# Kernel tuning notes

Measured on AMD Instinct MI355X. Metric: run time of the kernel, lower is better.

## Reference

```python
import jax, jax.numpy as jnp
import numpy as np

N_NODES = 50000
N_EDGES = 800000
IN_F = 128
H_F = 128
OUT_F = 128
N_GRAPHS = 128


def setup_inputs() -> dict:
    key = jax.random.key(0)
    ks = jax.random.split(key, 7)
    x = jax.random.normal(ks[0], (N_NODES, IN_F), dtype=jnp.float32)
    edge_index = jax.random.randint(ks[1], (2, N_EDGES), 0, N_NODES, dtype=jnp.int32)
    batch = jnp.sort(jax.random.randint(ks[2], (N_NODES,), 0, N_GRAPHS, dtype=jnp.int32))
    s1 = 1.0 / np.sqrt(IN_F)
    s2 = 1.0 / np.sqrt(H_F)
    W1 = jax.random.uniform(ks[3], (IN_F, H_F), jnp.float32, -s1, s1)
    b1 = jnp.zeros((H_F,), jnp.float32)
    W2 = jax.random.uniform(ks[4], (H_F, OUT_F), jnp.float32, -s2, s2)
    b2 = jnp.zeros((OUT_F,), jnp.float32)
    return {"x": x, "edge_index": edge_index, "batch": batch,
            "W1": W1, "b1": b1, "W2": W2, "b2": b2}


def _gcn_conv(x, W, b, src, dst, n_nodes):
    # PyG GCNConv: out = D^{-1/2} (A + I) D^{-1/2} (x W) + b
    h = x @ W  # [N, out]
    # degree including self-loop
    deg = jax.ops.segment_sum(jnp.ones_like(dst, dtype=h.dtype), dst,
                              num_segments=n_nodes) + 1.0
    dinv = jax.lax.rsqrt(deg)  # [N]
    norm = dinv[src] * dinv[dst]  # [E]
    agg = jax.ops.segment_sum(h[src] * norm[:, None], dst, num_segments=n_nodes)
    # self-loop term has norm dinv[i]^2
    return agg + (dinv * dinv)[:, None] * h + b


def reference(x, edge_index, batch, W1, b1, W2, b2):
    src, dst = edge_index[0], edge_index[1]
    h = jax.nn.relu(_gcn_conv(x, W1, b1, src, dst, N_NODES))
    h = _gcn_conv(h, W2, b2, src, dst, N_NODES)
    # global_add_pool over graphs
    return jax.ops.segment_sum(h, batch, num_segments=N_GRAPHS)
```

## Files before the change

### kernel.cpp

```cpp
#include <hip/hip_runtime.h>
#include <hip/hip_bf16.h>


typedef _Float16 f16x8 __attribute__((ext_vector_type(8)));
typedef float f32x4 __attribute__((ext_vector_type(4)));

#define BCHUNK 4096

static __device__ __forceinline__ float f16lo(unsigned int u) {
    union { unsigned short s; _Float16 h; } c; c.s = (unsigned short)(u & 0xffff);
    return (float)c.h;
}
static __device__ __forceinline__ float f16hi(unsigned int u) {
    union { unsigned short s; _Float16 h; } c; c.s = (unsigned short)(u >> 16);
    return (float)c.h;
}
static __device__ __forceinline__ unsigned int pack2f16(float x, float y) {
    union { unsigned short s; _Float16 h; } a, b;
    a.h = (_Float16)x; b.h = (_Float16)y;
    return (unsigned int)a.s | ((unsigned int)b.s << 16);
}


__global__ __launch_bounds__(256) void bin_hist(const int* __restrict__ ei,
                                                int* __restrict__ counts,
                                                int E, int NB, int NBLK) {
    __shared__ int hist[256];
    int t = threadIdx.x, blk = blockIdx.x;
    for (int b = t; b < NB; b += 256) hist[b] = 0;
    __syncthreads();
    int base = blk * BCHUNK;
    int end = min(E, base + BCHUNK);
    for (int e = base + t; e < end; e += 256)
        atomicAdd(&hist[ei[E + e] >> 8], 1);
    __syncthreads();
    for (int b = t; b < NB; b += 256) counts[b * NBLK + blk] = hist[b];
}

__global__ __launch_bounds__(256) void bin_scatter(const int* __restrict__ ei,
                                                   const int* __restrict__ counts,
                                                   unsigned int* __restrict__ bedges,
                                                   int E, int NB, int NBLK) {
    __shared__ int lcur[256];
    int t = threadIdx.x, blk = blockIdx.x;
    for (int b = t; b < NB; b += 256) lcur[b] = counts[b * NBLK + blk];
    __syncthreads();
    int base = blk * BCHUNK;
    int end = min(E, base + BCHUNK);
    for (int e = base + t; e < end; e += 256) {
        int s = ei[e];
        int d = ei[E + e];
        int pos = atomicAdd(&lcur[d >> 8], 1);
        bedges[pos] = (unsigned int)s | ((unsigned int)(d & 255) << 16);
    }
}

__global__ __launch_bounds__(256) void deg_buckets(const unsigned int* __restrict__ bedges,
                                                   const int* __restrict__ counts,
                                                   int* __restrict__ cnt,
                                                   int E, int N, int NB, int NBLK) {
    __shared__ int lcnt[256];
    int b = blockIdx.x, t = threadIdx.x;
    lcnt[t] = 0;
    __syncthreads();
    int bstart = counts[b * NBLK];
    int bend = (b + 1 < NB) ? counts[(b + 1) * NBLK] : E;
    for (int i = bstart + t; i < bend; i += 256)
        atomicAdd(&lcnt[bedges[i] >> 16], 1);
    __syncthreads();
    int node = (b << 8) + t;
    if (node < N) cnt[node] = lcnt[t];
}

__global__ __launch_bounds__(256) void fill_buckets(const unsigned int* __restrict__ bedges,
                                                    const int* __restrict__ counts,
                                                    const int* __restrict__ row_start,
                                                    int* __restrict__ srcs,
                                                    int E, int N, int NB, int NBLK) {
    __shared__ int lcur[256];
    int b = blockIdx.x, t = threadIdx.x;
    int node = (b << 8) + t;
    lcur[t] = (node < N) ? row_start[node] : 0;
    __syncthreads();
    int bstart = counts[b * NBLK];
    int bend = (b + 1 < NB) ? counts[(b + 1) * NBLK] : E;
    for (int i = bstart + t; i < bend; i += 256) {
        unsigned int p = bedges[i];
        int pos = atomicAdd(&lcur[p >> 16], 1);
        srcs[pos] = (int)(p & 0xffffu);
    }
}


__global__ void block_sums(const int* __restrict__ data, int* __restrict__ bsum, int n) {
    __shared__ int s[256];
    int base = blockIdx.x * 1024;
    int t = threadIdx.x;
    int v = 0;
#pragma unroll
    for (int i = 0; i < 4; i++) {
        int idx = base + t * 4 + i;
        if (idx < n) v += data[idx];
    }
    s[t] = v;
    __syncthreads();
    for (int off = 128; off > 0; off >>= 1) {
        if (t < off) s[t] += s[t + off];
        __syncthreads();
    }
    if (t == 0) bsum[blockIdx.x] = s[0];
}

__global__ void scan_bsum(int* __restrict__ bsum, int nb) {
    int lane = threadIdx.x & 63;
    int v = (lane < nb) ? bsum[lane] : 0;
    int incl = v;
#pragma unroll
    for (int off = 1; off < 64; off *= 2) {
        int u = __shfl_up(incl, off);
        if (lane >= off) incl += u;
    }
    if (lane < nb) bsum[lane] = incl - v;
}

__global__ void scan_apply(int* __restrict__ data, const int* __restrict__ bsum, int n) {
    __shared__ int s[256];
    int base = blockIdx.x * 1024;
    int t = threadIdx.x;
    int loc[4];
    int v = 0;
#pragma unroll
    for (int i = 0; i < 4; i++) {
        int idx = base + t * 4 + i;
        loc[i] = (idx < n) ? data[idx] : 0;
        v += loc[i];
    }
    s[t] = v;
    __syncthreads();
    for (int off = 1; off < 256; off *= 2) {
        int u = (t >= off) ? s[t - off] : 0;
        __syncthreads();
        s[t] += u;
        __syncthreads();
    }
    int excl = s[t] - v + bsum[blockIdx.x];
#pragma unroll
    for (int i = 0; i < 4; i++) {
        int idx = base + t * 4 + i;
        if (idx < n) { data[idx] = excl; excl += loc[i]; }
    }
}

__global__ void scan_nodes(const int* __restrict__ cnt, const int* __restrict__ bsum,
                           int* __restrict__ row_start, float* __restrict__ dinv, int n) {
    __shared__ int s[256];
    int base = blockIdx.x * 1024;
    int t = threadIdx.x;
    int loc[4];
    int v = 0;
#pragma unroll
    for (int i = 0; i < 4; i++) {
        int idx = base + t * 4 + i;
        loc[i] = (idx < n) ? cnt[idx] : 0;
        v += loc[i];
    }
    s[t] = v;
    __syncthreads();
    for (int off = 1; off < 256; off *= 2) {
        int u = (t >= off) ? s[t - off] : 0;
        __syncthreads();
        s[t] += u;
        __syncthreads();
    }
    int excl = s[t] - v + bsum[blockIdx.x];
#pragma unroll
    for (int i = 0; i < 4; i++) {
        int idx = base + t * 4 + i;
        if (idx < n) {
            row_start[idx] = excl;
            dinv[idx] = rsqrtf((float)loc[i] + 1.0f);
            excl += loc[i];
        }
    }
}

__global__ void wprep(const float* __restrict__ W, _Float16* __restrict__ wfrag) {
    int idx = blockIdx.x * 256 + threadIdx.x;
    if (idx >= 2048) return;
    int lane = idx & 63;
    int kc = (idx >> 6) & 3;
    int nb = idx >> 8;
    int col = nb * 16 + (lane & 15);
    int krow = kc * 32 + (lane >> 4) * 8;
#pragma unroll
    for (int j = 0; j < 8; j++)
        wfrag[idx * 8 + j] = (_Float16)W[(krow + j) * 128 + col];
}

template <bool A_IS_F32>
__global__ __launch_bounds__(256) void gemm_mfma(const void* __restrict__ Av,
                                                 const _Float16* __restrict__ wfrag,
                                                 _Float16* __restrict__ C, int M) {
    __shared__ _Float16 As[128 * 136];
    int t = threadIdx.x;
    int row0 = blockIdx.x * 128;

    if (A_IS_F32) {
        const float4* A4 = (const float4*)Av;
#pragma unroll
        for (int it = 0; it < 16; it++) {
            int v = it * 256 + t;
            int row = v >> 5;
            int seg = v & 31;
            float4 val = make_float4(0.f, 0.f, 0.f, 0.f);
            if (row0 + row < M) val = A4[(size_t)(row0 + row) * 32 + seg];
            _Float16* p = &As[row * 136 + seg * 4];
            p[0] = (_Float16)val.x; p[1] = (_Float16)val.y;
            p[2] = (_Float16)val.z; p[3] = (_Float16)val.w;
        }
    } else {
        const uint4* A4 = (const uint4*)Av;
#pragma unroll
        for (int it = 0; it < 8; it++) {
            int v = it * 256 + t;
            int row = v >> 4;
            int seg = v & 15;
            uint4 val = make_uint4(0, 0, 0, 0);
            if (row0 + row < M) val = A4[(size_t)(row0 + row) * 16 + seg];
            *((uint4*)&As[row * 136 + seg * 8]) = val;
        }
    }
    __syncthreads();

    int wv = t >> 6;
    int lane = t & 63;
    int lrow = lane & 15;
    int lq = lane >> 4;

    f32x4 acc[2][8];
#pragma unroll
    for (int i = 0; i < 2; i++)
#pragma unroll
        for (int j = 0; j < 8; j++) acc[i][j] = (f32x4){0.f, 0.f, 0.f, 0.f};

#pragma unroll
    for (int kc = 0; kc < 4; kc++) {
        int k0 = kc * 32;
        f16x8 a0 = *((const f16x8*)&As[(wv * 32 + lrow) * 136 + k0 + lq * 8]);
        f16x8 a1 = *((const f16x8*)&As[(wv * 32 + 16 + lrow) * 136 + k0 + lq * 8]);
#pragma unroll
        for (int nb = 0; nb < 8; nb++) {
            f16x8 b = ((const f16x8*)wfrag)[(nb * 4 + kc) * 64 + lane];
            acc[0][nb] = __builtin_amdgcn_mfma_f32_16x16x32_f16(a0, b, acc[0][nb], 0, 0, 0);
            acc[1][nb] = __builtin_amdgcn_mfma_f32_16x16x32_f16(a1, b, acc[1][nb], 0, 0, 0);
        }
    }

#pragma unroll
    for (int ti = 0; ti < 2; ti++) {
#pragma unroll
        for (int r = 0; r < 4; r++) {
            int row = row0 + wv * 32 + ti * 16 + lq * 4 + r;
            if (row < M) {
#pragma unroll
                for (int nb = 0; nb < 8; nb++)
                    C[(size_t)row * 128 + nb * 16 + lrow] = (_Float16)acc[ti][nb][r];
            }
        }
    }
}

template <bool RELU>
__global__ __launch_bounds__(256) void agg(const _Float16* __restrict__ hb,
                                           const int* __restrict__ srcs,
                                           const int* __restrict__ row_start,
                                           const int* __restrict__ cnt,
                                           const float* __restrict__ dinv,
                                           const float* __restrict__ bias,
                                           _Float16* __restrict__ ob, int n) {
    int node = blockIdx.x * 4 + (threadIdx.x >> 6);
    if (node >= n) return;
    int lane = threadIdx.x & 63;
    int s0 = row_start[node];
    int c = cnt[node];
    float dn = dinv[node];
    const unsigned int* h2 = (const unsigned int*)hb;
    float ax = 0.f, ay = 0.f, bx = 0.f, by = 0.f;
    int e = 0;
    for (; e + 8 <= c; e += 8) {
        int s0i = srcs[s0 + e + 0];
        int s1i = srcs[s0 + e + 1];
        int s2i = srcs[s0 + e + 2];
        int s3i = srcs[s0 + e + 3];
        int s4i = srcs[s0 + e + 4];
        int s5i = srcs[s0 + e + 5];
        int s6i = srcs[s0 + e + 6];
        int s7i = srcs[s0 + e + 7];
        float d0 = dinv[s0i], d1 = dinv[s1i], d2 = dinv[s2i], d3 = dinv[s3i];
        float d4 = dinv[s4i], d5 = dinv[s5i], d6 = dinv[s6i], d7 = dinv[s7i];
        unsigned int v0 = h2[(size_t)s0i * 64 + lane];
        unsigned int v1 = h2[(size_t)s1i * 64 + lane];
        unsigned int v2 = h2[(size_t)s2i * 64 + lane];
        unsigned int v3 = h2[(size_t)s3i * 64 + lane];
        unsigned int v4 = h2[(size_t)s4i * 64 + lane];
        unsigned int v5 = h2[(size_t)s5i * 64 + lane];
        unsigned int v6 = h2[(size_t)s6i * 64 + lane];
        unsigned int v7 = h2[(size_t)s7i * 64 + lane];
        float w0 = d0 * dn, w1 = d1 * dn, w2 = d2 * dn, w3 = d3 * dn;
        float w4 = d4 * dn, w5 = d5 * dn, w6 = d6 * dn, w7 = d7 * dn;
        ax = fmaf(w0, f16lo(v0), ax); ay = fmaf(w0, f16hi(v0), ay);
        bx = fmaf(w1, f16lo(v1), bx); by = fmaf(w1, f16hi(v1), by);
        ax = fmaf(w2, f16lo(v2), ax); ay = fmaf(w2, f16hi(v2), ay);
        bx = fmaf(w3, f16lo(v3), bx); by = fmaf(w3, f16hi(v3), by);
        ax = fmaf(w4, f16lo(v4), ax); ay = fmaf(w4, f16hi(v4), ay);
        bx = fmaf(w5, f16lo(v5), bx); by = fmaf(w5, f16hi(v5), by);
        ax = fmaf(w6, f16lo(v6), ax); ay = fmaf(w6, f16hi(v6), ay);
        bx = fmaf(w7, f16lo(v7), bx); by = fmaf(w7, f16hi(v7), by);
    }
    for (; e + 4 <= c; e += 4) {
        int s0i = srcs[s0 + e + 0];
        int s1i = srcs[s0 + e + 1];
        int s2i = srcs[s0 + e + 2];
        int s3i = srcs[s0 + e + 3];
        float d0 = dinv[s0i], d1 = dinv[s1i], d2 = dinv[s2i], d3 = dinv[s3i];
        unsigned int v0 = h2[(size_t)s0i * 64 + lane];
        unsigned int v1 = h2[(size_t)s1i * 64 + lane];
        unsigned int v2 = h2[(size_t)s2i * 64 + lane];
        unsigned int v3 = h2[(size_t)s3i * 64 + lane];
        float w0 = d0 * dn, w1 = d1 * dn, w2 = d2 * dn, w3 = d3 * dn;
        ax = fmaf(w0, f16lo(v0), ax); ay = fmaf(w0, f16hi(v0), ay);
        bx = fmaf(w1, f16lo(v1), bx); by = fmaf(w1, f16hi(v1), by);
        ax = fmaf(w2, f16lo(v2), ax); ay = fmaf(w2, f16hi(v2), ay);
        bx = fmaf(w3, f16lo(v3), bx); by = fmaf(w3, f16hi(v3), by);
    }
    for (; e < c; e++) {
        int si = srcs[s0 + e];
        float w = dinv[si] * dn;
        unsigned int v = h2[(size_t)si * 64 + lane];
        ax = fmaf(w, f16lo(v), ax); ay = fmaf(w, f16hi(v), ay);
    }
    ax += bx; ay += by;
    float sw = dn * dn;
    unsigned int hs = h2[(size_t)node * 64 + lane];
    float2 bv = ((const float2*)bias)[lane];
    float ox = ax + sw * f16lo(hs) + bv.x;
    float oy = ay + sw * f16hi(hs) + bv.y;
    if (RELU) { ox = fmaxf(ox, 0.f); oy = fmaxf(oy, 0.f); }
    ((unsigned int*)ob)[(size_t)node * 64 + lane] = pack2f16(ox, oy);
}

#define POOL_CHUNK 128
__global__ __launch_bounds__(256) void pool2h(const _Float16* __restrict__ feat,
                                              const int* __restrict__ batch,
                                              float* __restrict__ out, int n) {
    int wave = threadIdx.x >> 6;
    int lane = threadIdx.x & 63;
    int base = blockIdx.x * POOL_CHUNK;
    int end = base + POOL_CHUNK;
    if (end > n) end = n;
    const unsigned int* f2 = (const unsigned int*)feat;
    float accx = 0.f, accy = 0.f;
    int cur_g = -1;
    for (int i = base + wave; i < end; i += 4) {
        int g = batch[i];
        if (g != cur_g) {
            if (cur_g >= 0) {
                atomicAdd(&out[cur_g * 128 + lane * 2 + 0], accx);
                atomicAdd(&out[cur_g * 128 + lane * 2 + 1], accy);
            }
            cur_g = g;
            accx = 0.f; accy = 0.f;
        }
        unsigned int v = f2[(size_t)i * 64 + lane];
        accx += f16lo(v);
        accy += f16hi(v);
    }
    if (cur_g >= 0) {
        atomicAdd(&out[cur_g * 128 + lane * 2 + 0], accx);
        atomicAdd(&out[cur_g * 128 + lane * 2 + 1], accy);
    }
}

extern "C" void kernel_launch(void* const* d_in, const int* in_sizes, int n_in,
                              void* d_out, int out_size, void* d_ws, size_t ws_size,
                              hipStream_t stream) {
    const float* x  = (const float*)d_in[0];
    const int*   ei = (const int*)d_in[1];
    const int*   batch = (const int*)d_in[2];
    const float* W1 = (const float*)d_in[3];
    const float* b1 = (const float*)d_in[4];
    const float* W2 = (const float*)d_in[5];
    const float* b2 = (const float*)d_in[6];
    float* out = (float*)d_out;

    const int N = in_sizes[2];
    const int E = in_sizes[1] / 2;

    const int NB = (N + 255) >> 8;
    const int NBLK = (E + BCHUNK - 1) / BCHUNK;
    const int ncounts = NB * NBLK;

    _Float16* hb = (_Float16*)d_ws;
    _Float16* ob = hb + (size_t)N * 128;
    int* cnt  = (int*)(ob + (size_t)N * 128);
    int* row_start = cnt + N;
    float* dinv    = (float*)(row_start + N);
    int* srcs      = (int*)(dinv + N);
    unsigned int* bedges = (unsigned int*)(srcs + E);
    int* counts    = (int*)(bedges + E);
    _Float16* wfrag1 = (_Float16*)(counts + ncounts);
    _Float16* wfrag2 = wfrag1 + 128 * 128;
    int* bsum      = (int*)(wfrag2 + 128 * 128);

    const int nbc = (ncounts + 1023) / 1024;
    const int nbn = (N + 1023) / 1024;

    hipMemsetAsync(out, 0, (size_t)out_size * sizeof(float), stream);
    wprep<<<8, 256, 0, stream>>>(W1, wfrag1);
    wprep<<<8, 256, 0, stream>>>(W2, wfrag2);

    bin_hist<<<NBLK, 256, 0, stream>>>(ei, counts, E, NB, NBLK);
    block_sums<<<nbc, 256, 0, stream>>>(counts, bsum, ncounts);
    scan_bsum<<<1, 64, 0, stream>>>(bsum, nbc);
    scan_apply<<<nbc, 256, 0, stream>>>(counts, bsum, ncounts);
    bin_scatter<<<NBLK, 256, 0, stream>>>(ei, counts, bedges, E, NB, NBLK);
    deg_buckets<<<NB, 256, 0, stream>>>(bedges, counts, cnt, E, N, NB, NBLK);
    block_sums<<<nbn, 256, 0, stream>>>(cnt, bsum, N);
    scan_bsum<<<1, 64, 0, stream>>>(bsum, nbn);
    scan_nodes<<<nbn, 256, 0, stream>>>(cnt, bsum, row_start, dinv, N);
    fill_buckets<<<NB, 256, 0, stream>>>(bedges, counts, row_start, srcs, E, N, NB, NBLK);

    const int gemm_grid = (N + 127) / 128;

    gemm_mfma<true><<<gemm_grid, 256, 0, stream>>>(x, wfrag1, hb, N);
    agg<true><<<(N + 3) / 4, 256, 0, stream>>>(hb, srcs, row_start, cnt, dinv, b1, ob, N);
    gemm_mfma<false><<<gemm_grid, 256, 0, stream>>>(ob, wfrag2, hb, N);
    agg<false><<<(N + 3) / 4, 256, 0, stream>>>(hb, srcs, row_start, cnt, dinv, b2, ob, N);
    pool2h<<<(N + POOL_CHUNK - 1) / POOL_CHUNK, 256, 0, stream>>>(ob, batch, out, N);
}
```

Measured before the change: 241.2 us.

## Reorder second GCN layer: aggregate and pool before applying W2

Exploits linearity of the second layer. It aggregates the layer-1 output over neighbours, pools per graph into a small 128x128 buffer, and only then multiplies by W2 and adds bias scaled by node count per graph. This removes the full N x 128 x 128 second GEMM and the separate pool pass, fusing aggregation with pooling. Pooling now uses block-level shared-memory reduction plus atomics. Accumulation happens in fp32 before the weight multiply, which slightly changes rounding order.

```diff
diff --git a/kernel.cpp b/kernel.cpp
--- a/kernel.cpp
+++ b/kernel.cpp
@@ -197,38 +197,24 @@
         wfrag[idx * 8 + j] = (_Float16)W[(krow + j) * 128 + col];
 }
 
-template <bool A_IS_F32>
-__global__ __launch_bounds__(256) void gemm_mfma(const void* __restrict__ Av,
-                                                 const _Float16* __restrict__ wfrag,
-                                                 _Float16* __restrict__ C, int M) {
+__global__ __launch_bounds__(256) void gemm_mfma_f32in(const float* __restrict__ A,
+                                                       const _Float16* __restrict__ wfrag,
+                                                       _Float16* __restrict__ C, int M) {
     __shared__ _Float16 As[128 * 136];
     int t = threadIdx.x;
     int row0 = blockIdx.x * 128;
 
-    if (A_IS_F32) {
-        const float4* A4 = (const float4*)Av;
-#pragma unroll
-        for (int it = 0; it < 16; it++) {
-            int v = it * 256 + t;
-            int row = v >> 5;
-            int seg = v & 31;
-            float4 val = make_float4(0.f, 0.f, 0.f, 0.f);
-            if (row0 + row < M) val = A4[(size_t)(row0 + row) * 32 + seg];
-            _Float16* p = &As[row * 136 + seg * 4];
-            p[0] = (_Float16)val.x; p[1] = (_Float16)val.y;
-            p[2] = (_Float16)val.z; p[3] = (_Float16)val.w;
-        }
-    } else {
-        const uint4* A4 = (const uint4*)Av;
-#pragma unroll
-        for (int it = 0; it < 8; it++) {
-            int v = it * 256 + t;
-            int row = v >> 4;
-            int seg = v & 15;
-            uint4 val = make_uint4(0, 0, 0, 0);
-            if (row0 + row < M) val = A4[(size_t)(row0 + row) * 16 + seg];
-            *((uint4*)&As[row * 136 + seg * 8]) = val;
-        }
+    const float4* A4 = (const float4*)A;
+#pragma unroll
+    for (int it = 0; it < 16; it++) {
+        int v = it * 256 + t;
+        int row = v >> 5;
+        int seg = v & 31;
+        float4 val = make_float4(0.f, 0.f, 0.f, 0.f);
+        if (row0 + row < M) val = A4[(size_t)(row0 + row) * 32 + seg];
+        _Float16* p = &As[row * 136 + seg * 4];
+        p[0] = (_Float16)val.x; p[1] = (_Float16)val.y;
+        p[2] = (_Float16)val.z; p[3] = (_Float16)val.w;
     }
     __syncthreads();
 
@@ -270,14 +256,13 @@
     }
 }
 
-template <bool RELU>
-__global__ __launch_bounds__(256) void agg(const _Float16* __restrict__ hb,
-                                           const int* __restrict__ srcs,
-                                           const int* __restrict__ row_start,
-                                           const int* __restrict__ cnt,
-                                           const float* __restrict__ dinv,
-                                           const float* __restrict__ bias,
-                                           _Float16* __restrict__ ob, int n) {
+__global__ __launch_bounds__(256) void agg1(const _Float16* __restrict__ hb,
+                                            const int* __restrict__ srcs,
+                                            const int* __restrict__ row_start,
+                                            const int* __restrict__ cnt,
+                                            const float* __restrict__ dinv,
+                                            const float* __restrict__ bias,
+                                            _Float16* __restrict__ ob, int n) {
     int node = blockIdx.x * 4 + (threadIdx.x >> 6);
     if (node >= n) return;
     int lane = threadIdx.x & 63;
@@ -345,40 +330,127 @@
     float2 bv = ((const float2*)bias)[lane];
     float ox = ax + sw * f16lo(hs) + bv.x;
     float oy = ay + sw * f16hi(hs) + bv.y;
-    if (RELU) { ox = fmaxf(ox, 0.f); oy = fmaxf(oy, 0.f); }
+    ox = fmaxf(ox, 0.f); oy = fmaxf(oy, 0.f);
     ((unsigned int*)ob)[(size_t)node * 64 + lane] = pack2f16(ox, oy);
 }
 
-#define POOL_CHUNK 128
-__global__ __launch_bounds__(256) void pool2h(const _Float16* __restrict__ feat,
-                                              const int* __restrict__ batch,
-                                              float* __restrict__ out, int n) {
-    int wave = threadIdx.x >> 6;
+__global__ __launch_bounds__(256) void agg2_pool(const _Float16* __restrict__ ob,
+                                                 const int* __restrict__ srcs,
+                                                 const int* __restrict__ row_start,
+                                                 const int* __restrict__ cnt,
+                                                 const float* __restrict__ dinv,
+                                                 const int* __restrict__ batch,
+                                                 float* __restrict__ P, int n) {
+    __shared__ float red[4][128];
+    int wv = threadIdx.x >> 6;
     int lane = threadIdx.x & 63;
-    int base = blockIdx.x * POOL_CHUNK;
-    int end = base + POOL_CHUNK;
-    if (end > n) end = n;
-    const unsigned int* f2 = (const unsigned int*)feat;
-    float accx = 0.f, accy = 0.f;
-    int cur_g = -1;
-    for (int i = base + wave; i < end; i += 4) {
-        int g = batch[i];
-        if (g != cur_g) {
-            if (cur_g >= 0) {
-                atomicAdd(&out[cur_g * 128 + lane * 2 + 0], accx);
-                atomicAdd(&out[cur_g * 128 + lane * 2 + 1], accy);
-            }
-            cur_g = g;
-            accx = 0.f; accy = 0.f;
-        }
-        unsigned int v = f2[(size_t)i * 64 + lane];
-        accx += f16lo(v);
-        accy += f16hi(v);
-    }
-    if (cur_g >= 0) {
-        atomicAdd(&out[cur_g * 128 + lane * 2 + 0], accx);
-        atomicAdd(&out[cur_g * 128 + lane * 2 + 1], accy);
-    }
+    int base = blockIdx.x * 4;
+    int node = base + wv;
+    const unsigned int* h2 = (const unsigned int*)ob;
+    float ax = 0.f, ay = 0.f, bx = 0.f, by = 0.f;
+    int g = -1;
+    if (node < n) {
+        g = batch[node];
+        int s0 = row_start[node];
+        int c = cnt[node];
+        float dn = dinv[node];
+        int e = 0;
+        for (; e + 8 <= c; e += 8) {
+            int s0i = srcs[s0 + e + 0];
+            int s1i = srcs[s0 + e + 1];
+            int s2i = srcs[s0 + e + 2];
+            int s3i = srcs[s0 + e + 3];
+            int s4i = srcs[s0 + e + 4];
+            int s5i = srcs[s0 + e + 5];
+            int s6i = srcs[s0 + e + 6];
+            int s7i = srcs[s0 + e + 7];
+            float d0 = dinv[s0i], d1 = dinv[s1i], d2 = dinv[s2i], d3 = dinv[s3i];
+            float d4 = dinv[s4i], d5 = dinv[s5i], d6 = dinv[s6i], d7 = dinv[s7i];
+            unsigned int v0 = h2[(size_t)s0i * 64 + lane];
+            unsigned int v1 = h2[(size_t)s1i * 64 + lane];
+            unsigned int v2 = h2[(size_t)s2i * 64 + lane];
+            unsigned int v3 = h2[(size_t)s3i * 64 + lane];
+            unsigned int v4 = h2[(size_t)s4i * 64 + lane];
+            unsigned int v5 = h2[(size_t)s5i * 64 + lane];
+            unsigned int v6 = h2[(size_t)s6i * 64 + lane];
+            unsigned int v7 = h2[(size_t)s7i * 64 + lane];
+            float w0 = d0 * dn, w1 = d1 * dn, w2 = d2 * dn, w3 = d3 * dn;
+            float w4 = d4 * dn, w5 = d5 * dn, w6 = d6 * dn, w7 = d7 * dn;
+            ax = fmaf(w0, f16lo(v0), ax); ay = fmaf(w0, f16hi(v0), ay);
+            bx = fmaf(w1, f16lo(v1), bx); by = fmaf(w1, f16hi(v1), by);
+            ax = fmaf(w2, f16lo(v2), ax); ay = fmaf(w2, f16hi(v2), ay);
+            bx = fmaf(w3, f16lo(v3), bx); by = fmaf(w3, f16hi(v3), by);
+            ax = fmaf(w4, f16lo(v4), ax); ay = fmaf(w4, f16hi(v4), ay);
+            bx = fmaf(w5, f16lo(v5), bx); by = fmaf(w5, f16hi(v5), by);
+            ax = fmaf(w6, f16lo(v6), ax); ay = fmaf(w6, f16hi(v6), ay);
+            bx = fmaf(w7, f16lo(v7), bx); by = fmaf(w7, f16hi(v7), by);
+        }
+        for (; e + 4 <= c; e += 4) {
+            int s0i = srcs[s0 + e + 0];
+            int s1i = srcs[s0 + e + 1];
+            int s2i = srcs[s0 + e + 2];
+            int s3i = srcs[s0 + e + 3];
+            float d0 = dinv[s0i], d1 = dinv[s1i], d2 = dinv[s2i], d3 = dinv[s3i];
+            unsigned int v0 = h2[(size_t)s0i * 64 + lane];
+            unsigned int v1 = h2[(size_t)s1i * 64 + lane];
+            unsigned int v2 = h2[(size_t)s2i * 64 + lane];
+            unsigned int v3 = h2[(size_t)s3i * 64 + lane];
+            float w0 = d0 * dn, w1 = d1 * dn, w2 = d2 * dn, w3 = d3 * dn;
+            ax = fmaf(w0, f16lo(v0), ax); ay = fmaf(w0, f16hi(v0), ay);
+            bx = fmaf(w1, f16lo(v1), bx); by = fmaf(w1, f16hi(v1), by);
+            ax = fmaf(w2, f16lo(v2), ax); ay = fmaf(w2, f16hi(v2), ay);
+            bx = fmaf(w3, f16lo(v3), bx); by = fmaf(w3, f16hi(v3), by);
+        }
+        for (; e < c; e++) {
+            int si = srcs[s0 + e];
+            float w = dinv[si] * dn;
+            unsigned int v = h2[(size_t)si * 64 + lane];
+            ax = fmaf(w, f16lo(v), ax); ay = fmaf(w, f16hi(v), ay);
+        }
+        ax += bx; ay += by;
+        float sw = dn * dn;
+        unsigned int hs = h2[(size_t)node * 64 + lane];
+        ax += sw * f16lo(hs);
+        ay += sw * f16hi(hs);
+    }
+    int lastn = min(base + 3, n - 1);
+    bool uniform = (base < n) && (batch[base] == batch[lastn]) && (base + 3 < n);
+    if (uniform) {
+        red[wv][lane * 2 + 0] = ax;
+        red[wv][lane * 2 + 1] = ay;
+        __syncthreads();
+        if (wv == 0) {
+            float sx = red[0][lane * 2] + red[1][lane * 2] + red[2][lane * 2] + red[3][lane * 2];
+            float sy = red[0][lane * 2 + 1] + red[1][lane * 2 + 1] + red[2][lane * 2 + 1] + red[3][lane * 2 + 1];
+            atomicAdd(&P[g * 128 + lane * 2 + 0], sx);
+            atomicAdd(&P[g * 128 + lane * 2 + 1], sy);
+        }
+    } else if (node < n) {
+        atomicAdd(&P[g * 128 + lane * 2 + 0], ax);
+        atomicAdd(&P[g * 128 + lane * 2 + 1], ay);
+    }
+}
+
+__global__ __launch_bounds__(128) void gemm_small(const float* __restrict__ P,
+                                                  const float* __restrict__ W2,
+                                                  const float* __restrict__ b2,
+                                                  const int* __restrict__ batch,
+                                                  float* __restrict__ out, int n) {
+    __shared__ float prow[128];
+    int g = blockIdx.x;
+    int c = threadIdx.x;
+    prow[c] = P[g * 128 + c];
+    __syncthreads();
+    int lo = 0, hi = n;
+    while (lo < hi) { int mid = (lo + hi) >> 1; if (batch[mid] < g) lo = mid + 1; else hi = mid; }
+    int start = lo;
+    hi = n;
+    while (lo < hi) { int mid = (lo + hi) >> 1; if (batch[mid] < g + 1) lo = mid + 1; else hi = mid; }
+    float ng = (float)(lo - start);
+    float acc = 0.f;
+#pragma unroll 8
+    for (int k = 0; k < 128; k++) acc = fmaf(prow[k], W2[k * 128 + c], acc);
+    out[g * 128 + c] = acc + ng * b2[c];
 }
 
 extern "C" void kernel_launch(void* const* d_in, const int* in_sizes, int n_in,
@@ -409,15 +481,14 @@
     unsigned int* bedges = (unsigned int*)(srcs + E);
     int* counts    = (int*)(bedges + E);
     _Float16* wfrag1 = (_Float16*)(counts + ncounts);
-    _Float16* wfrag2 = wfrag1 + 128 * 128;
-    int* bsum      = (int*)(wfrag2 + 128 * 128);
+    float* P       = (float*)(wfrag1 + 128 * 128);
+    int* bsum      = (int*)(P + 128 * 128);
 
     const int nbc = (ncounts + 1023) / 1024;
     const int nbn = (N + 1023) / 1024;
 
-    hipMemsetAsync(out, 0, (size_t)out_size * sizeof(float), stream);
+    hipMemsetAsync(P, 0, 128 * 128 * sizeof(float), stream);
     wprep<<<8, 256, 0, stream>>>(W1, wfrag1);
-    wprep<<<8, 256, 0, stream>>>(W2, wfrag2);
 
     bin_hist<<<NBLK, 256, 0, stream>>>(ei, counts, E, NB, NBLK);
     block_sums<<<nbc, 256, 0, stream>>>(counts, bsum, ncounts);
@@ -432,9 +503,8 @@
 
     const int gemm_grid = (N + 127) / 128;
 
-    gemm_mfma<true><<<gemm_grid, 256, 0, stream>>>(x, wfrag1, hb, N);
-    agg<true><<<(N + 3) / 4, 256, 0, stream>>>(hb, srcs, row_start, cnt, dinv, b1, ob, N);
-    gemm_mfma<false><<<gemm_grid, 256, 0, stream>>>(ob, wfrag2, hb, N);
-    agg<false><<<(N + 3) / 4, 256, 0, stream>>>(hb, srcs, row_start, cnt, dinv, b2, ob, N);
-    pool2h<<<(N + POOL_CHUNK - 1) / POOL_CHUNK, 256, 0, stream>>>(ob, batch, out, N);
-}
+    gemm_mfma_f32in<<<gemm_grid, 256, 0, stream>>>(x, wfrag1, hb, N);
+    agg1<<<(N + 3) / 4, 256, 0, stream>>>(hb, srcs, row_start, cnt, dinv, b1, ob, N);
+    agg2_pool<<<(N + 3) / 4, 256, 0, stream>>>(ob, srcs, row_start, cnt, dinv, batch, P, N);
+    gemm_small<<<128, 128, 0, stream>>>(P, W2, b2, batch, out, N);
+}
```

Result: faster. 235.9 us (-2.2%).

## Reorder layer-2 GEMM after pooling and slice features for cache-local aggregation

Applied to the files above, without the earlier changes.

Uses linearity to move the second layer's weight multiply after global pooling: layer-2 aggregation now runs on the 128-wide hidden features and is pooled per graph directly, then a small 128x128 GEMM applies W2 and adds the bias scaled by each graph's node count. The first GEMM pre-scales rows by dinv and writes a feature-sliced layout (8 slices of 16 features), so each aggregation block gathers only a 32-byte slice per edge, aiming for better L2 locality. This removes the large second GEMM, the separate pooling kernel and one full feature-matrix round trip. In exchange it adds atomics per graph slice and binary searches over the batch array, and it assumes the batch array is sorted.

```diff
diff --git a/kernel.cpp b/kernel.cpp
--- a/kernel.cpp
+++ b/kernel.cpp
@@ -197,38 +197,25 @@
         wfrag[idx * 8 + j] = (_Float16)W[(krow + j) * 128 + col];
 }
 
-template <bool A_IS_F32>
-__global__ __launch_bounds__(256) void gemm_mfma(const void* __restrict__ Av,
-                                                 const _Float16* __restrict__ wfrag,
-                                                 _Float16* __restrict__ C, int M) {
+__global__ __launch_bounds__(256) void gemm_mfma_f32in(const float* __restrict__ A,
+                                                       const _Float16* __restrict__ wfrag,
+                                                       const float* __restrict__ dinv,
+                                                       _Float16* __restrict__ C, int M) {
     __shared__ _Float16 As[128 * 136];
     int t = threadIdx.x;
     int row0 = blockIdx.x * 128;
 
-    if (A_IS_F32) {
-        const float4* A4 = (const float4*)Av;
-#pragma unroll
-        for (int it = 0; it < 16; it++) {
-            int v = it * 256 + t;
-            int row = v >> 5;
-            int seg = v & 31;
-            float4 val = make_float4(0.f, 0.f, 0.f, 0.f);
-            if (row0 + row < M) val = A4[(size_t)(row0 + row) * 32 + seg];
-            _Float16* p = &As[row * 136 + seg * 4];
-            p[0] = (_Float16)val.x; p[1] = (_Float16)val.y;
-            p[2] = (_Float16)val.z; p[3] = (_Float16)val.w;
-        }
-    } else {
-        const uint4* A4 = (const uint4*)Av;
-#pragma unroll
-        for (int it = 0; it < 8; it++) {
-            int v = it * 256 + t;
-            int row = v >> 4;
-            int seg = v & 15;
-            uint4 val = make_uint4(0, 0, 0, 0);
-            if (row0 + row < M) val = A4[(size_t)(row0 + row) * 16 + seg];
-            *((uint4*)&As[row * 136 + seg * 8]) = val;
-        }
+    const float4* A4 = (const float4*)A;
+#pragma unroll
+    for (int it = 0; it < 16; it++) {
+        int v = it * 256 + t;
+        int row = v >> 5;
+        int seg = v & 31;
+        float4 val = make_float4(0.f, 0.f, 0.f, 0.f);
+        if (row0 + row < M) val = A4[(size_t)(row0 + row) * 32 + seg];
+        _Float16* p = &As[row * 136 + seg * 4];
+        p[0] = (_Float16)val.x; p[1] = (_Float16)val.y;
+        p[2] = (_Float16)val.z; p[3] = (_Float16)val.w;
     }
     __syncthreads();
 
@@ -262,123 +249,112 @@
         for (int r = 0; r < 4; r++) {
             int row = row0 + wv * 32 + ti * 16 + lq * 4 + r;
             if (row < M) {
+                float sc = dinv[row];
 #pragma unroll
                 for (int nb = 0; nb < 8; nb++)
-                    C[(size_t)row * 128 + nb * 16 + lrow] = (_Float16)acc[ti][nb][r];
+                    C[((size_t)nb * M + row) * 16 + lrow] = (_Float16)(acc[ti][nb][r] * sc);
             }
         }
     }
 }
 
-template <bool RELU>
-__global__ __launch_bounds__(256) void agg(const _Float16* __restrict__ hb,
-                                           const int* __restrict__ srcs,
-                                           const int* __restrict__ row_start,
-                                           const int* __restrict__ cnt,
-                                           const float* __restrict__ dinv,
-                                           const float* __restrict__ bias,
-                                           _Float16* __restrict__ ob, int n) {
-    int node = blockIdx.x * 4 + (threadIdx.x >> 6);
-    if (node >= n) return;
+template <bool L1>
+__global__ __launch_bounds__(256) void agg_sliced(const _Float16* __restrict__ tab,
+                                                  const int* __restrict__ srcs,
+                                                  const int* __restrict__ row_start,
+                                                  const int* __restrict__ cnt,
+                                                  const float* __restrict__ dinv,
+                                                  const float* __restrict__ bias,
+                                                  const int* __restrict__ batch,
+                                                  _Float16* __restrict__ obout,
+                                                  float* __restrict__ P, int N) {
+    int j = blockIdx.x & 7;
+    int grp = blockIdx.x >> 3;
+    int wv = threadIdx.x >> 6;
     int lane = threadIdx.x & 63;
-    int s0 = row_start[node];
-    int c = cnt[node];
-    float dn = dinv[node];
-    const unsigned int* h2 = (const unsigned int*)hb;
-    float ax = 0.f, ay = 0.f, bx = 0.f, by = 0.f;
-    int e = 0;
-    for (; e + 8 <= c; e += 8) {
-        int s0i = srcs[s0 + e + 0];
-        int s1i = srcs[s0 + e + 1];
-        int s2i = srcs[s0 + e + 2];
-        int s3i = srcs[s0 + e + 3];
-        int s4i = srcs[s0 + e + 4];
-        int s5i = srcs[s0 + e + 5];
-        int s6i = srcs[s0 + e + 6];
-        int s7i = srcs[s0 + e + 7];
-        float d0 = dinv[s0i], d1 = dinv[s1i], d2 = dinv[s2i], d3 = dinv[s3i];
-        float d4 = dinv[s4i], d5 = dinv[s5i], d6 = dinv[s6i], d7 = dinv[s7i];
-        unsigned int v0 = h2[(size_t)s0i * 64 + lane];
-        unsigned int v1 = h2[(size_t)s1i * 64 + lane];
-        unsigned int v2 = h2[(size_t)s2i * 64 + lane];
-        unsigned int v3 = h2[(size_t)s3i * 64 + lane];
-        unsigned int v4 = h2[(size_t)s4i * 64 + lane];
-        unsigned int v5 = h2[(size_t)s5i * 64 + lane];
-        unsigned int v6 = h2[(size_t)s6i * 64 + lane];
-        unsigned int v7 = h2[(size_t)s7i * 64 + lane];
-        float w0 = d0 * dn, w1 = d1 * dn, w2 = d2 * dn, w3 = d3 * dn;
-        float w4 = d4 * dn, w5 = d5 * dn, w6 = d6 * dn, w7 = d7 * dn;
-        ax = fmaf(w0, f16lo(v0), ax); ay = fmaf(w0, f16hi(v0), ay);
-        bx = fmaf(w1, f16lo(v1), bx); by = fmaf(w1, f16hi(v1), by);
-        ax = fmaf(w2, f16lo(v2), ax); ay = fmaf(w2, f16hi(v2), ay);
-        bx = fmaf(w3, f16lo(v3), bx); by = fmaf(w3, f16hi(v3), by);
-        ax = fmaf(w4, f16lo(v4), ax); ay = fmaf(w4, f16hi(v4), ay);
-        bx = fmaf(w5, f16lo(v5), bx); by = fmaf(w5, f16hi(v5), by);
-        ax = fmaf(w6, f16lo(v6), ax); ay = fmaf(w6, f16hi(v6), ay);
-        bx = fmaf(w7, f16lo(v7), bx); by = fmaf(w7, f16hi(v7), by);
-    }
-    for (; e + 4 <= c; e += 4) {
-        int s0i = srcs[s0 + e + 0];
-        int s1i = srcs[s0 + e + 1];
-        int s2i = srcs[s0 + e + 2];
-        int s3i = srcs[s0 + e + 3];
-        float d0 = dinv[s0i], d1 = dinv[s1i], d2 = dinv[s2i], d3 = dinv[s3i];
-        unsigned int v0 = h2[(size_t)s0i * 64 + lane];
-        unsigned int v1 = h2[(size_t)s1i * 64 + lane];
-        unsigned int v2 = h2[(size_t)s2i * 64 + lane];
-        unsigned int v3 = h2[(size_t)s3i * 64 + lane];
-        float w0 = d0 * dn, w1 = d1 * dn, w2 = d2 * dn, w3 = d3 * dn;
-        ax = fmaf(w0, f16lo(v0), ax); ay = fmaf(w0, f16hi(v0), ay);
-        bx = fmaf(w1, f16lo(v1), bx); by = fmaf(w1, f16hi(v1), by);
-        ax = fmaf(w2, f16lo(v2), ax); ay = fmaf(w2, f16hi(v2), ay);
-        bx = fmaf(w3, f16lo(v3), bx); by = fmaf(w3, f16hi(v3), by);
-    }
-    for (; e < c; e++) {
-        int si = srcs[s0 + e];
-        float w = dinv[si] * dn;
-        unsigned int v = h2[(size_t)si * 64 + lane];
-        ax = fmaf(w, f16lo(v), ax); ay = fmaf(w, f16hi(v), ay);
-    }
-    ax += bx; ay += by;
-    float sw = dn * dn;
-    unsigned int hs = h2[(size_t)node * 64 + lane];
-    float2 bv = ((const float2*)bias)[lane];
-    float ox = ax + sw * f16lo(hs) + bv.x;
-    float oy = ay + sw * f16hi(hs) + bv.y;
-    if (RELU) { ox = fmaxf(ox, 0.f); oy = fmaxf(oy, 0.f); }
-    ((unsigned int*)ob)[(size_t)node * 64 + lane] = pack2f16(ox, oy);
-}
-
-#define POOL_CHUNK 128
-__global__ __launch_bounds__(256) void pool2h(const _Float16* __restrict__ feat,
-                                              const int* __restrict__ batch,
-                                              float* __restrict__ out, int n) {
-    int wave = threadIdx.x >> 6;
-    int lane = threadIdx.x & 63;
-    int base = blockIdx.x * POOL_CHUNK;
-    int end = base + POOL_CHUNK;
-    if (end > n) end = n;
-    const unsigned int* f2 = (const unsigned int*)feat;
-    float accx = 0.f, accy = 0.f;
-    int cur_g = -1;
-    for (int i = base + wave; i < end; i += 4) {
-        int g = batch[i];
-        if (g != cur_g) {
-            if (cur_g >= 0) {
-                atomicAdd(&out[cur_g * 128 + lane * 2 + 0], accx);
-                atomicAdd(&out[cur_g * 128 + lane * 2 + 1], accy);
+    int fg = lane & 7;
+    int eg = lane >> 3;
+    const unsigned int* T = (const unsigned int*)tab + (size_t)j * N * 8;
+    float2 bv = make_float2(0.f, 0.f);
+    if (L1) bv = ((const float2*)bias)[j * 8 + fg];
+    float ppx = 0.f, ppy = 0.f;
+    int curg = -1;
+    int nbase = grp * 16 + wv * 4;
+    for (int k = 0; k < 4; k++) {
+        int node = nbase + k;
+        if (node >= N) break;
+        int s0 = row_start[node];
+        int c = cnt[node];
+        float dn = dinv[node];
+        float ax = 0.f, ay = 0.f;
+        for (int e = 0; e <= c; e += 8) {
+            int idx = e + eg;
+            int si = (idx < c) ? srcs[s0 + idx] : node;
+            float m = (idx <= c) ? 1.f : 0.f;
+            unsigned int v = T[(size_t)si * 8 + fg];
+            ax = fmaf(m, f16lo(v), ax);
+            ay = fmaf(m, f16hi(v), ay);
+        }
+        if (L1) {
+            ax += __shfl_xor(ax, 8);  ay += __shfl_xor(ay, 8);
+            ax += __shfl_xor(ax, 16); ay += __shfl_xor(ay, 16);
+            ax += __shfl_xor(ax, 32); ay += __shfl_xor(ay, 32);
+            float ox = dn * fmaxf(fmaf(dn, ax, bv.x), 0.f);
+            float oy = dn * fmaxf(fmaf(dn, ay, bv.y), 0.f);
+            if (eg == 0)
+                ((unsigned int*)obout)[((size_t)j * N + node) * 8 + fg] = pack2f16(ox, oy);
+        } else {
+            int g = batch[node];
+            if (g != curg) {
+                if (curg >= 0) {
+                    float sx = ppx, sy = ppy;
+                    sx += __shfl_xor(sx, 8);  sy += __shfl_xor(sy, 8);
+                    sx += __shfl_xor(sx, 16); sy += __shfl_xor(sy, 16);
+                    sx += __shfl_xor(sx, 32); sy += __shfl_xor(sy, 32);
+                    if (eg == 0) {
+                        atomicAdd(&P[curg * 128 + j * 16 + fg * 2 + 0], sx);
+                        atomicAdd(&P[curg * 128 + j * 16 + fg * 2 + 1], sy);
+                    }
+                }
+                curg = g;
+                ppx = 0.f; ppy = 0.f;
             }
-            cur_g = g;
-            accx = 0.f; accy = 0.f;
-        }
-        unsigned int v = f2[(size_t)i * 64 + lane];
-        accx += f16lo(v);
-        accy += f16hi(v);
-    }
-    if (cur_g >= 0) {
-        atomicAdd(&out[cur_g * 128 + lane * 2 + 0], accx);
-        atomicAdd(&out[cur_g * 128 + lane * 2 + 1], accy);
-    }
+            ppx = fmaf(dn, ax, ppx);
+            ppy = fmaf(dn, ay, ppy);
+        }
+    }
+    if (!L1 && curg >= 0) {
+        float sx = ppx, sy = ppy;
+        sx += __shfl_xor(sx, 8);  sy += __shfl_xor(sy, 8);
+        sx += __shfl_xor(sx, 16); sy += __shfl_xor(sy, 16);
+        sx += __shfl_xor(sx, 32); sy += __shfl_xor(sy, 32);
+        if (eg == 0) {
+            atomicAdd(&P[curg * 128 + j * 16 + fg * 2 + 0], sx);
+            atomicAdd(&P[curg * 128 + j * 16 + fg * 2 + 1], sy);
+        }
+    }
+}
+
+__global__ __launch_bounds__(128) void gemm_small(const float* __restrict__ P,
+                                                  const float* __restrict__ W2,
+                                                  const float* __restrict__ b2,
+                                                  const int* __restrict__ batch,
+                                                  float* __restrict__ out, int n) {
+    __shared__ float prow[128];
+    int g = blockIdx.x;
+    int c = threadIdx.x;
+    prow[c] = P[g * 128 + c];
+    __syncthreads();
+    int lo = 0, hi = n;
+    while (lo < hi) { int mid = (lo + hi) >> 1; if (batch[mid] < g) lo = mid + 1; else hi = mid; }
+    int start = lo;
+    hi = n;
+    while (lo < hi) { int mid = (lo + hi) >> 1; if (batch[mid] < g + 1) lo = mid + 1; else hi = mid; }
+    float ng = (float)(lo - start);
+    float acc = 0.f;
+#pragma unroll 8
+    for (int k = 0; k < 128; k++) acc = fmaf(prow[k], W2[k * 128 + c], acc);
+    out[g * 128 + c] = acc + ng * b2[c];
 }
 
 extern "C" void kernel_launch(void* const* d_in, const int* in_sizes, int n_in,
@@ -409,15 +385,14 @@
     unsigned int* bedges = (unsigned int*)(srcs + E);
     int* counts    = (int*)(bedges + E);
     _Float16* wfrag1 = (_Float16*)(counts + ncounts);
-    _Float16* wfrag2 = wfrag1 + 128 * 128;
-    int* bsum      = (int*)(wfrag2 + 128 * 128);
+    float* P       = (float*)(wfrag1 + 128 * 128);
+    int* bsum      = (int*)(P + 128 * 128);
 
     const int nbc = (ncounts + 1023) / 1024;
     const int nbn = (N + 1023) / 1024;
 
-    hipMemsetAsync(out, 0, (size_t)out_size * sizeof(float), stream);
+    hipMemsetAsync(P, 0, 128 * 128 * sizeof(float), stream);
     wprep<<<8, 256, 0, stream>>>(W1, wfrag1);
-    wprep<<<8, 256, 0, stream>>>(W2, wfrag2);
 
     bin_hist<<<NBLK, 256, 0, stream>>>(ei, counts, E, NB, NBLK);
     block_sums<<<nbc, 256, 0, stream>>>(counts, bsum, ncounts);
@@ -431,10 +406,12 @@
     fill_buckets<<<NB, 256, 0, stream>>>(bedges, counts, row_start, srcs, E, N, NB, NBLK);
 
     const int gemm_grid = (N + 127) / 128;
-
-    gemm_mfma<true><<<gemm_grid, 256, 0, stream>>>(x, wfrag1, hb, N);
-    agg<true><<<(N + 3) / 4, 256, 0, stream>>>(hb, srcs, row_start, cnt, dinv, b1, ob, N);
-    gemm_mfma<false><<<gemm_grid, 256, 0, stream>>>(ob, wfrag2, hb, N);
-    agg<false><<<(N + 3) / 4, 256, 0, stream>>>(hb, srcs, row_start, cnt, dinv, b2, ob, N);
-    pool2h<<<(N + POOL_CHUNK - 1) / POOL_CHUNK, 256, 0, stream>>>(ob, batch, out, N);
-}
+    const int agg_grid = ((N + 15) / 16) * 8;
+
+    gemm_mfma_f32in<<<gemm_grid, 256, 0, stream>>>(x, wfrag1, dinv, hb, N);
+    agg_sliced<true><<<agg_grid, 256, 0, stream>>>(hb, srcs, row_start, cnt, dinv, b1,
+                                                   nullptr, ob, nullptr, N);
+    agg_sliced<false><<<agg_grid, 256, 0, stream>>>(ob, srcs, row_start, cnt, dinv, nullptr,
+                                                    batch, nullptr, P, N);
+    gemm_small<<<128, 128, 0, stream>>>(P, W2, b2, batch, out, N);
+}
```

Result: slower. 379.2 us (+57.2%).
